# Optimization experiments

Measured on AMD Instinct MI355X. Metric: run time of the kernel, lower is better.

The kernel has to match this reference:

```python
import jax, jax.numpy as jnp
import numpy as np

N_HEADS = 8
D_HEAD = 64
SCALE = D_HEAD ** -0.5


def setup_inputs() -> dict:
    key = jax.random.key(0)
    k1, k2, k3 = jax.random.split(key, 3)
    B, H, W, C = 16, 32, 32, 512
    ft = jax.random.normal(k1, (B, H, W, C), dtype=jnp.float32)
    # Dense layers: to_qkv -> n_heads*n_dim_heads*3 = 1536 units, to_out -> n_channels
    w_qkv = jax.random.normal(k2, (C, N_HEADS * D_HEAD * 3), dtype=jnp.float32) * (C ** -0.5)
    b_qkv = jnp.zeros((N_HEADS * D_HEAD * 3,), dtype=jnp.float32)
    w_out = jax.random.normal(k3, (N_HEADS * D_HEAD, C), dtype=jnp.float32) * ((N_HEADS * D_HEAD) ** -0.5)
    b_out = jnp.zeros((C,), dtype=jnp.float32)
    return {"ft": ft, "w_qkv": w_qkv, "b_qkv": b_qkv, "w_out": w_out, "b_out": b_out}


def reference(ft, w_qkv, b_qkv, w_out, b_out):
    B, H, W, C = ft.shape
    N = H * W
    x = ft.reshape(B, N, C)                       # b (h w) c
    qkv = x @ w_qkv + b_qkv                       # b n (heads * 3*d_head)
    qkv = qkv.reshape(B, N, N_HEADS, 3 * D_HEAD)  # 'b x (h d) -> b x h d'
    q, k, v = jnp.split(qkv, 3, axis=-1)          # each: b n heads d_head
    attn = jnp.einsum('bxhd,byhd->bxyh', q, k) * SCALE
    attn = jax.nn.softmax(attn, axis=2)           # softmax over key axis y
    res = jnp.einsum('bxyh,byhd->bxhd', attn, v)  # b x h d
    res = res.reshape(B, N, N_HEADS * D_HEAD)     # 'b x h d -> b x (h d)'
    res = res @ w_out + b_out
    res = res + x                                 # residual with pre-qkv flattened input
    return res.reshape(B, H, W, C)
```

## Files before the change

kernel.cpp:

```cpp
#include <hip/hip_runtime.h>
#include <hip/hip_bf16.h>

using u16 = unsigned short;
using u32 = unsigned int;
typedef __attribute__((ext_vector_type(8))) short short8;
typedef __attribute__((ext_vector_type(4))) float f32x4;

#define MFMA16(A, B, C) __builtin_amdgcn_mfma_f32_16x16x32_bf16((A), (B), (C), 0, 0, 0)

__device__ __forceinline__ u16 f2bf(float f) {
  union { float f; u32 i; } v; v.f = f;
  u32 x = v.i;
  return (u16)((x + 0x7fffu + ((x >> 16) & 1u)) >> 16);
}
__device__ __forceinline__ u32 pkbf(float a, float b) {
  union { __hip_bfloat162 h; u32 u; } v;
  v.h = __float22bfloat162_rn(make_float2(a, b));
  return v.u;
}
__device__ __forceinline__ void gl16(const u16* g, u16* l) {
  __builtin_amdgcn_global_load_lds(
      (const __attribute__((address_space(1))) u32*)g,
      (__attribute__((address_space(3))) u32*)l, 16, 0, 0);
}

__global__ __launch_bounds__(256) void conv_x(const float* __restrict__ X,
                                              u16* __restrict__ Xbf) {
  const int i = (blockIdx.x * 256 + threadIdx.x) * 8;
  float4 a = *(const float4*)(X + i);
  float4 b = *(const float4*)(X + i + 4);
  uint4 o;
  o.x = pkbf(a.x, a.y); o.y = pkbf(a.z, a.w);
  o.z = pkbf(b.x, b.y); o.w = pkbf(b.z, b.w);
  *(uint4*)(Xbf + i) = o;
}

__global__ __launch_bounds__(256) void transpose_w(
    const float* __restrict__ Wq, const float* __restrict__ Wo,
    u16* __restrict__ Wqt, u16* __restrict__ Wot) {
  const int z = blockIdx.z;
  if (z == 1 && blockIdx.x >= 16) return;
  const float* src = z ? Wo : Wq;
  u16* dst = z ? Wot : Wqt;
  const int ncols = z ? 512 : 1536;
  __shared__ float tile[32][33];
  const int t = threadIdx.x;
  const int kt = blockIdx.y * 32, nt = blockIdx.x * 32;
  const int r = t >> 3, c4 = (t & 7) * 4;
  float4 v = *(const float4*)(src + (size_t)(kt + r) * ncols + nt + c4);
  tile[r][c4 + 0] = v.x; tile[r][c4 + 1] = v.y;
  tile[r][c4 + 2] = v.z; tile[r][c4 + 3] = v.w;
  __syncthreads();
  uint2 p = make_uint2(pkbf(tile[c4 + 0][r], tile[c4 + 1][r]),
                       pkbf(tile[c4 + 2][r], tile[c4 + 3][r]));
  *(uint2*)(dst + (size_t)(nt + r) * 512 + kt + c4) = p;
}

__global__ __launch_bounds__(256) void qkv_gemm(
    const u16* __restrict__ Xbf, const u16* __restrict__ Wt,
    const float* __restrict__ Bias,
    u16* __restrict__ Qp, u16* __restrict__ Kp, u16* __restrict__ Vt) {
  __shared__ u16 Xs[128][32];
  __shared__ u16 Ws[128][32];
  const int t = threadIdx.x;
  const int bm = blockIdx.y * 128, bn = blockIdx.x * 128;
  const int w = t >> 6, lane = t & 63, quad = lane >> 4, l16 = lane & 15;
  const int mtb = (w >> 1) * 64, ntb = (w & 1) * 64;
  const int rr = lane >> 2;
  const int gch = ((lane & 3) ^ ((lane >> 3) & 3)) * 8;
  const int sw = (quad ^ ((l16 >> 1) & 3)) * 8;

  const u16* xg0 = Xbf + (size_t)(bm + w * 16 + rr) * 512 + gch;
  const u16* xg1 = xg0 + (size_t)64 * 512;
  const u16* wg0 = Wt + (size_t)(bn + w * 16 + rr) * 512 + gch;
  const u16* wg1 = wg0 + (size_t)64 * 512;
  u16* xl0 = &Xs[w * 16][0]; u16* xl1 = &Xs[64 + w * 16][0];
  u16* wl0 = &Ws[w * 16][0]; u16* wl1 = &Ws[64 + w * 16][0];

  f32x4 acc[4][4];
  const f32x4 z4 = {0.f, 0.f, 0.f, 0.f};
  #pragma unroll
  for (int mi = 0; mi < 4; mi++)
    #pragma unroll
    for (int ni = 0; ni < 4; ni++) acc[mi][ni] = z4;

  for (int k0 = 0; k0 < 512; k0 += 32) {
    gl16(xg0 + k0, xl0);
    gl16(xg1 + k0, xl1);
    gl16(wg0 + k0, wl0);
    gl16(wg1 + k0, wl1);
    __syncthreads();
    short8 af[4], bf4[4];
    #pragma unroll
    for (int mi = 0; mi < 4; mi++)
      af[mi] = *(const short8*)&Xs[mtb + mi * 16 + l16][sw];
    #pragma unroll
    for (int ni = 0; ni < 4; ni++)
      bf4[ni] = *(const short8*)&Ws[ntb + ni * 16 + l16][sw];
    #pragma unroll
    for (int mi = 0; mi < 4; mi++)
      #pragma unroll
      for (int ni = 0; ni < 4; ni++)
        acc[mi][ni] = MFMA16(af[mi], bf4[ni], acc[mi][ni]);
    __syncthreads();
  }

  #pragma unroll
  for (int ni = 0; ni < 4; ni++) {
    const int g = bn + ntb + ni * 16;
    const int h = g / 192, rm = g % 192;
    const int type = rm >> 6, dbase = rm & 63;
    const float bias = Bias[g + l16];
    const float qsc = (type == 0) ? 0.125f : 1.0f;
    #pragma unroll
    for (int mi = 0; mi < 4; mi++) {
      const int row0 = bm + mtb + mi * 16 + quad * 4;
      const int b = row0 >> 10, n0 = row0 & 1023;
      const size_t bh = (size_t)(b * 8 + h) * 65536;
      if (type == 2) {
        uint2 p = make_uint2(pkbf(acc[mi][ni][0] + bias, acc[mi][ni][1] + bias),
                             pkbf(acc[mi][ni][2] + bias, acc[mi][ni][3] + bias));
        *(uint2*)(Vt + bh + (size_t)(dbase + l16) * 1024 + n0) = p;
      } else {
        u16* dst = (type ? Kp : Qp) + bh;
        #pragma unroll
        for (int r = 0; r < 4; r++)
          dst[(size_t)(n0 + r) * 64 + dbase + l16] =
              f2bf((acc[mi][ni][r] + bias) * qsc);
      }
    }
  }
}

__global__ __launch_bounds__(512, 4) void attn_mfma(
    const u16* __restrict__ Qp, const u16* __restrict__ Kp,
    const u16* __restrict__ Vt, u16* __restrict__ ATT) {
  __shared__ u16 Ks[128][72];
  __shared__ u16 Vs[64][136];
  __shared__ u16 Ps[128][136];
  const int t = threadIdx.x, w = t >> 6, lane = t & 63;
  const int quad = lane >> 4, l16 = lane & 15;
  const int bx = blockIdx.x;
  const int c = bx & 7, g = bx >> 3;
  const int qt = g & 7, u = g >> 3;
  const int bh_id = u * 8 + c;
  const int b = bh_id >> 3, h = bh_id & 7;
  const size_t bh = (size_t)bh_id * 65536;
  const u16* Qb = Qp + bh;
  const u16* Kb = Kp + bh;
  const u16* Vb = Vt + bh;
  const int q0 = qt * 128 + w * 16;

  const int kkey = t >> 2, koff = (t & 3) * 16;
  const int vrow = t >> 3, voff = (t & 7) * 16;
  const u16* Kg = Kb + (size_t)kkey * 64 + koff;
  const u16* Vg = Vb + (size_t)vrow * 1024 + voff;

  short8 qf[2];
  #pragma unroll
  for (int ks = 0; ks < 2; ks++)
    qf[ks] = *(const short8*)(Qb + (size_t)(q0 + l16) * 64 + ks * 32 + quad * 8);

  float m_ = -1e30f, l_ = 0.f;
  f32x4 Of[4];
  const f32x4 z4 = {0.f, 0.f, 0.f, 0.f};
  #pragma unroll
  for (int ni = 0; ni < 4; ni++) Of[ni] = z4;

  uint4 kr0 = *(const uint4*)(Kg);
  uint4 kr1 = *(const uint4*)(Kg + 8);
  uint4 vr0 = *(const uint4*)(Vg);
  uint4 vr1 = *(const uint4*)(Vg + 8);

  for (int kt = 0; kt < 8; kt++) {
    __syncthreads();
    *(uint4*)&Ks[kkey][koff]     = kr0;
    *(uint4*)&Ks[kkey][koff + 8] = kr1;
    *(uint4*)&Vs[vrow][voff]     = vr0;
    *(uint4*)&Vs[vrow][voff + 8] = vr1;
    if (kt < 7) {
      kr0 = *(const uint4*)(Kg + (kt + 1) * 8192);
      kr1 = *(const uint4*)(Kg + (kt + 1) * 8192 + 8);
      vr0 = *(const uint4*)(Vg + (kt + 1) * 128);
      vr1 = *(const uint4*)(Vg + (kt + 1) * 128 + 8);
    }
    __syncthreads();

    f32x4 s[8];
    #pragma unroll
    for (int nt = 0; nt < 8; nt++) s[nt] = z4;
    #pragma unroll
    for (int nt = 0; nt < 8; nt++) {
      short8 k0f = *(const short8*)&Ks[nt * 16 + l16][quad * 8];
      short8 k1f = *(const short8*)&Ks[nt * 16 + l16][quad * 8 + 32];
      s[nt] = MFMA16(k0f, qf[0], s[nt]);
      s[nt] = MFMA16(k1f, qf[1], s[nt]);
    }
    float mloc = -1e30f;
    #pragma unroll
    for (int nt = 0; nt < 8; nt++)
      #pragma unroll
      for (int r = 0; r < 4; r++) mloc = fmaxf(mloc, s[nt][r]);
    mloc = fmaxf(mloc, __shfl_xor(mloc, 16));
    mloc = fmaxf(mloc, __shfl_xor(mloc, 32));
    const float mnew = fmaxf(m_, mloc);
    const float alpha = __expf(m_ - mnew);
    float rs = 0.f;
    #pragma unroll
    for (int nt = 0; nt < 8; nt++) {
      float p0 = __expf(s[nt][0] - mnew), p1 = __expf(s[nt][1] - mnew);
      float p2 = __expf(s[nt][2] - mnew), p3 = __expf(s[nt][3] - mnew);
      rs += (p0 + p1) + (p2 + p3);
      *(uint2*)&Ps[w * 16 + l16][nt * 16 + quad * 4] =
          make_uint2(pkbf(p0, p1), pkbf(p2, p3));
    }
    rs += __shfl_xor(rs, 16);
    rs += __shfl_xor(rs, 32);
    l_ = l_ * alpha + rs;
    m_ = mnew;
    float av[4];
    #pragma unroll
    for (int r = 0; r < 4; r++) av[r] = __shfl(alpha, quad * 4 + r);
    #pragma unroll
    for (int ni = 0; ni < 4; ni++)
      #pragma unroll
      for (int r = 0; r < 4; r++) Of[ni][r] *= av[r];
    #pragma unroll
    for (int ks = 0; ks < 4; ks++) {
      short8 pa = *(const short8*)&Ps[w * 16 + l16][ks * 32 + quad * 8];
      #pragma unroll
      for (int ni = 0; ni < 4; ni++) {
        short8 vf = *(const short8*)&Vs[ni * 16 + l16][ks * 32 + quad * 8];
        Of[ni] = MFMA16(pa, vf, Of[ni]);
      }
    }
  }
  float lv[4];
  #pragma unroll
  for (int r = 0; r < 4; r++) lv[r] = __shfl(l_, quad * 4 + r);
  #pragma unroll
  for (int r = 0; r < 4; r++) {
    const float inv = 1.0f / lv[r];
    const int row = b * 1024 + q0 + quad * 4 + r;
    #pragma unroll
    for (int ni = 0; ni < 4; ni++)
      ATT[(size_t)row * 512 + h * 64 + ni * 16 + l16] = f2bf(Of[ni][r] * inv);
  }
}

__global__ __launch_bounds__(256) void out_proj(
    const u16* __restrict__ A, const u16* __restrict__ Wt,
    const float* __restrict__ Bias, const float* __restrict__ FT,
    float* __restrict__ OUT) {
  __shared__ u16 As[128][32];
  __shared__ u16 Ws[128][32];
  const int t = threadIdx.x;
  const int bm = blockIdx.y * 128, bn = blockIdx.x * 128;
  const int w = t >> 6, lane = t & 63, quad = lane >> 4, l16 = lane & 15;
  const int mtb = (w >> 1) * 64, ntb = (w & 1) * 64;
  const int rr = lane >> 2;
  const int gch = ((lane & 3) ^ ((lane >> 3) & 3)) * 8;
  const int sw = (quad ^ ((l16 >> 1) & 3)) * 8;

  const u16* ag0 = A + (size_t)(bm + w * 16 + rr) * 512 + gch;
  const u16* ag1 = ag0 + (size_t)64 * 512;
  const u16* wg0 = Wt + (size_t)(bn + w * 16 + rr) * 512 + gch;
  const u16* wg1 = wg0 + (size_t)64 * 512;
  u16* al0 = &As[w * 16][0]; u16* al1 = &As[64 + w * 16][0];
  u16* wl0 = &Ws[w * 16][0]; u16* wl1 = &Ws[64 + w * 16][0];

  f32x4 acc[4][4];
  const f32x4 z4 = {0.f, 0.f, 0.f, 0.f};
  #pragma unroll
  for (int mi = 0; mi < 4; mi++)
    #pragma unroll
    for (int ni = 0; ni < 4; ni++) acc[mi][ni] = z4;

  for (int k0 = 0; k0 < 512; k0 += 32) {
    gl16(ag0 + k0, al0);
    gl16(ag1 + k0, al1);
    gl16(wg0 + k0, wl0);
    gl16(wg1 + k0, wl1);
    __syncthreads();
    short8 af[4], bf4[4];
    #pragma unroll
    for (int mi = 0; mi < 4; mi++)
      af[mi] = *(const short8*)&As[mtb + mi * 16 + l16][sw];
    #pragma unroll
    for (int ni = 0; ni < 4; ni++)
      bf4[ni] = *(const short8*)&Ws[ntb + ni * 16 + l16][sw];
    #pragma unroll
    for (int mi = 0; mi < 4; mi++)
      #pragma unroll
      for (int ni = 0; ni < 4; ni++)
        acc[mi][ni] = MFMA16(af[mi], bf4[ni], acc[mi][ni]);
    __syncthreads();
  }

  #pragma unroll
  for (int ni = 0; ni < 4; ni++) {
    const int g = bn + ntb + ni * 16;
    const float bias = Bias[g + l16];
    #pragma unroll
    for (int mi = 0; mi < 4; mi++) {
      const int row0 = bm + mtb + mi * 16 + quad * 4;
      #pragma unroll
      for (int r = 0; r < 4; r++) {
        const size_t idx = (size_t)(row0 + r) * 512 + g + l16;
        OUT[idx] = acc[mi][ni][r] + bias + FT[idx];
      }
    }
  }
}

extern "C" void kernel_launch(void* const* d_in, const int* in_sizes, int n_in,
                              void* d_out, int out_size, void* d_ws, size_t ws_size,
                              hipStream_t stream) {
  const float* ft    = (const float*)d_in[0];
  const float* w_qkv = (const float*)d_in[1];
  const float* b_qkv = (const float*)d_in[2];
  const float* w_out = (const float*)d_in[3];
  const float* b_out = (const float*)d_in[4];
  float* out = (float*)d_out;

  char* p = (char*)d_ws;
  u16* Xbf    = (u16*)(p);
  u16* ATT    = Xbf;
  u16* Wqkv_t = (u16*)(p + 16777216);
  u16* Wout_t = (u16*)(p + 18350080);
  u16* Qp     = (u16*)(p + 18874368);
  u16* Kp     = (u16*)(p + 35651584);
  u16* Vt     = (u16*)(p + 52428800);

  conv_x     <<<4096, 256, 0, stream>>>(ft, Xbf);
  transpose_w<<<dim3(48, 16, 2), 256, 0, stream>>>(w_qkv, w_out, Wqkv_t, Wout_t);
  qkv_gemm   <<<dim3(12, 128), 256, 0, stream>>>(Xbf, Wqkv_t, b_qkv, Qp, Kp, Vt);
  attn_mfma  <<<dim3(1024), 512, 0, stream>>>(Qp, Kp, Vt, ATT);
  out_proj   <<<dim3(4, 128), 256, 0, stream>>>(ATT, Wout_t, b_out, ft, out);
}
```

Before: 219.2 us.

## Transpose Q store, stage K epilogue through LDS, swizzle P tile, use exp2

The QKV GEMM epilogue now writes Q transposed, like V, using packed 8-byte stores. K rows are staged through a swizzled LDS scratch so they leave as coalesced 16-byte stores instead of scattered 2-byte writes. The Q scale folds in log2(e) so attention can use exp2f instead of __expf. The P tile in attention gets an XOR swizzle to avoid LDS bank conflicts. The trade-off is that Q fragments are now loaded with 16 strided scalar loads per thread, and the K epilogue reuses Xs without a barrier, relying on per-wave regions.

```diff
diff --git a/kernel.cpp b/kernel.cpp
--- a/kernel.cpp
+++ b/kernel.cpp
@@ -7,6 +7,7 @@
 typedef __attribute__((ext_vector_type(4))) float f32x4;
 
 #define MFMA16(A, B, C) __builtin_amdgcn_mfma_f32_16x16x32_bf16((A), (B), (C), 0, 0, 0)
+#define QSCALE 0.18033688011112042f
 
 __device__ __forceinline__ u16 f2bf(float f) {
   union { float f; u32 i; } v; v.f = f;
@@ -59,7 +60,7 @@
 __global__ __launch_bounds__(256) void qkv_gemm(
     const u16* __restrict__ Xbf, const u16* __restrict__ Wt,
     const float* __restrict__ Bias,
-    u16* __restrict__ Qp, u16* __restrict__ Kp, u16* __restrict__ Vt) {
+    u16* __restrict__ Qt, u16* __restrict__ Kp, u16* __restrict__ Vt) {
   __shared__ u16 Xs[128][32];
   __shared__ u16 Ws[128][32];
   const int t = threadIdx.x;
@@ -105,39 +106,63 @@
     __syncthreads();
   }
 
-  #pragma unroll
-  for (int ni = 0; ni < 4; ni++) {
-    const int g = bn + ntb + ni * 16;
-    const int h = g / 192, rm = g % 192;
-    const int type = rm >> 6, dbase = rm & 63;
-    const float bias = Bias[g + l16];
-    const float qsc = (type == 0) ? 0.125f : 1.0f;
+  const int gcol0 = bn + ntb;
+  const int h = gcol0 / 192, rm = gcol0 % 192;
+  const int type = rm >> 6;
+
+  if (type != 1) {
+    u16* base = (type == 0) ? Qt : Vt;
+    const float sc = (type == 0) ? QSCALE : 1.0f;
+    #pragma unroll
+    for (int ni = 0; ni < 4; ni++) {
+      const float bias = Bias[gcol0 + ni * 16 + l16];
+      #pragma unroll
+      for (int mi = 0; mi < 4; mi++) {
+        const int row0 = bm + mtb + mi * 16 + quad * 4;
+        const int b = row0 >> 10, n0 = row0 & 1023;
+        const size_t bho = (size_t)(b * 8 + h) * 65536;
+        f32x4 a = acc[mi][ni];
+        uint2 p = make_uint2(pkbf((a[0] + bias) * sc, (a[1] + bias) * sc),
+                             pkbf((a[2] + bias) * sc, (a[3] + bias) * sc));
+        *(uint2*)(base + bho + (size_t)(ni * 16 + l16) * 1024 + n0) = p;
+      }
+    }
+  } else {
+    u16* scr = &Xs[0][0] + w * 1024;
     #pragma unroll
     for (int mi = 0; mi < 4; mi++) {
-      const int row0 = bm + mtb + mi * 16 + quad * 4;
-      const int b = row0 >> 10, n0 = row0 & 1023;
-      const size_t bh = (size_t)(b * 8 + h) * 65536;
-      if (type == 2) {
-        uint2 p = make_uint2(pkbf(acc[mi][ni][0] + bias, acc[mi][ni][1] + bias),
-                             pkbf(acc[mi][ni][2] + bias, acc[mi][ni][3] + bias));
-        *(uint2*)(Vt + bh + (size_t)(dbase + l16) * 1024 + n0) = p;
-      } else {
-        u16* dst = (type ? Kp : Qp) + bh;
+      #pragma unroll
+      for (int ni = 0; ni < 4; ni++) {
+        const float bias = Bias[gcol0 + ni * 16 + l16];
+        const int col = ni * 16 + l16;
         #pragma unroll
-        for (int r = 0; r < 4; r++)
-          dst[(size_t)(n0 + r) * 64 + dbase + l16] =
-              f2bf((acc[mi][ni][r] + bias) * qsc);
-      }
+        for (int r = 0; r < 4; r++) {
+          const int row = quad * 4 + r;
+          scr[row * 64 + ((((col >> 3) ^ (row & 7)) << 3) | (col & 7))] =
+              f2bf(acc[mi][ni][r] + bias);
+        }
+      }
+      __asm__ volatile("s_waitcnt lgkmcnt(0)" ::: "memory");
+      const int row0 = bm + mtb + mi * 16 + l16;
+      const int b = row0 >> 10, n0r = row0 & 1023;
+      const size_t bho = (size_t)(b * 8 + h) * 65536;
+      #pragma unroll
+      for (int i = 0; i < 2; i++) {
+        const int chunk = 2 * quad + i;
+        uint4 v = *(const uint4*)&scr[l16 * 64 + ((chunk ^ (l16 & 7)) << 3)];
+        *(uint4*)(Kp + bho + (size_t)n0r * 64 + chunk * 8) = v;
+      }
+      __asm__ volatile("s_waitcnt lgkmcnt(0)" ::: "memory");
     }
   }
 }
 
 __global__ __launch_bounds__(512, 4) void attn_mfma(
-    const u16* __restrict__ Qp, const u16* __restrict__ Kp,
+    const u16* __restrict__ Qt, const u16* __restrict__ Kp,
     const u16* __restrict__ Vt, u16* __restrict__ ATT) {
   __shared__ u16 Ks[128][72];
   __shared__ u16 Vs[64][136];
-  __shared__ u16 Ps[128][136];
+  __shared__ u16 Ps[128 * 128];
   const int t = threadIdx.x, w = t >> 6, lane = t & 63;
   const int quad = lane >> 4, l16 = lane & 15;
   const int bx = blockIdx.x;
@@ -146,7 +171,7 @@
   const int bh_id = u * 8 + c;
   const int b = bh_id >> 3, h = bh_id & 7;
   const size_t bh = (size_t)bh_id * 65536;
-  const u16* Qb = Qp + bh;
+  const u16* Qb = Qt + bh;
   const u16* Kb = Kp + bh;
   const u16* Vb = Vt + bh;
   const int q0 = qt * 128 + w * 16;
@@ -158,8 +183,13 @@
 
   short8 qf[2];
   #pragma unroll
-  for (int ks = 0; ks < 2; ks++)
-    qf[ks] = *(const short8*)(Qb + (size_t)(q0 + l16) * 64 + ks * 32 + quad * 8);
+  for (int ks = 0; ks < 2; ks++) {
+    short8 v;
+    #pragma unroll
+    for (int j = 0; j < 8; j++)
+      v[j] = (short)Qb[(size_t)(ks * 32 + quad * 8 + j) * 1024 + q0 + l16];
+    qf[ks] = v;
+  }
 
   float m_ = -1e30f, l_ = 0.f;
   f32x4 Of[4];
@@ -204,14 +234,15 @@
     mloc = fmaxf(mloc, __shfl_xor(mloc, 16));
     mloc = fmaxf(mloc, __shfl_xor(mloc, 32));
     const float mnew = fmaxf(m_, mloc);
-    const float alpha = __expf(m_ - mnew);
+    const float alpha = exp2f(m_ - mnew);
     float rs = 0.f;
     #pragma unroll
     for (int nt = 0; nt < 8; nt++) {
-      float p0 = __expf(s[nt][0] - mnew), p1 = __expf(s[nt][1] - mnew);
-      float p2 = __expf(s[nt][2] - mnew), p3 = __expf(s[nt][3] - mnew);
+      float p0 = exp2f(s[nt][0] - mnew), p1 = exp2f(s[nt][1] - mnew);
+      float p2 = exp2f(s[nt][2] - mnew), p3 = exp2f(s[nt][3] - mnew);
       rs += (p0 + p1) + (p2 + p3);
-      *(uint2*)&Ps[w * 16 + l16][nt * 16 + quad * 4] =
+      const int physW = (2 * nt + (quad >> 1)) ^ (l16 & 7);
+      *(uint2*)&Ps[(w * 16 + l16) * 128 + (physW << 3) + (quad & 1) * 4] =
           make_uint2(pkbf(p0, p1), pkbf(p2, p3));
     }
     rs += __shfl_xor(rs, 16);
@@ -227,7 +258,8 @@
       for (int r = 0; r < 4; r++) Of[ni][r] *= av[r];
     #pragma unroll
     for (int ks = 0; ks < 4; ks++) {
-      short8 pa = *(const short8*)&Ps[w * 16 + l16][ks * 32 + quad * 8];
+      const int physR = (4 * ks + quad) ^ (l16 & 7);
+      short8 pa = *(const short8*)&Ps[(w * 16 + l16) * 128 + (physR << 3)];
       #pragma unroll
       for (int ni = 0; ni < 4; ni++) {
         short8 vf = *(const short8*)&Vs[ni * 16 + l16][ks * 32 + quad * 8];
@@ -328,13 +360,13 @@
   u16* ATT    = Xbf;
   u16* Wqkv_t = (u16*)(p + 16777216);
   u16* Wout_t = (u16*)(p + 18350080);
-  u16* Qp     = (u16*)(p + 18874368);
+  u16* Qt     = (u16*)(p + 18874368);
   u16* Kp     = (u16*)(p + 35651584);
   u16* Vt     = (u16*)(p + 52428800);
 
   conv_x     <<<4096, 256, 0, stream>>>(ft, Xbf);
   transpose_w<<<dim3(48, 16, 2), 256, 0, stream>>>(w_qkv, w_out, Wqkv_t, Wout_t);
-  qkv_gemm   <<<dim3(12, 128), 256, 0, stream>>>(Xbf, Wqkv_t, b_qkv, Qp, Kp, Vt);
-  attn_mfma  <<<dim3(1024), 512, 0, stream>>>(Qp, Kp, Vt, ATT);
+  qkv_gemm   <<<dim3(12, 128), 256, 0, stream>>>(Xbf, Wqkv_t, b_qkv, Qt, Kp, Vt);
+  attn_mfma  <<<dim3(1024), 512, 0, stream>>>(Qt, Kp, Vt, ATT);
   out_proj   <<<dim3(4, 128), 256, 0, stream>>>(ATT, Wout_t, b_out, ft, out);
 }
```

Result: slower. 231.5 us (+5.6%).
